# Optimization experiments

Hardware: AMD Instinct MI355X
Metric: run time of the kernel (lower is better)

Reference implementation:

```python
import jax, jax.numpy as jnp
import numpy as np
from jax import lax

B, Ht, Wt, C, NH, KV, FF = 32, 32, 32, 768, 12, 16, 4
HD = C // NH
EPS = 1e-5


def setup_inputs() -> dict:
    key = jax.random.key(0)
    ks = jax.random.split(key, 12)
    rn = lambda k, s, sc=0.02: jax.random.normal(k, s, jnp.float32) * sc
    inp = {"x": jax.random.normal(ks[0], (B, Ht * Wt, C), jnp.float32)}
    inp["ln1_g"] = jnp.ones((C,), jnp.float32)
    inp["ln1_b"] = jnp.zeros((C,), jnp.float32)
    for i, nm in enumerate(["q", "k", "v"]):
        inp[f"dw_w_{nm}"] = rn(ks[1 + i], (C, 1, 3, 3), 0.1)
        inp[f"dw_b_{nm}"] = jnp.zeros((C,), jnp.float32)
        inp[f"bn_g_{nm}"] = jnp.ones((C,), jnp.float32)
        inp[f"bn_b_{nm}"] = jnp.zeros((C,), jnp.float32)
        inp[f"bn_m_{nm}"] = jnp.zeros((C,), jnp.float32)
        inp[f"bn_v_{nm}"] = jnp.ones((C,), jnp.float32)
        inp[f"W_{nm}"] = rn(ks[4 + i], (C, C))
        inp[f"b_{nm}"] = jnp.zeros((C,), jnp.float32)
    inp["ln2_g"] = jnp.ones((C,), jnp.float32)
    inp["ln2_b"] = jnp.zeros((C,), jnp.float32)
    inp["W1"] = rn(ks[7], (FF * C, C))
    inp["b1"] = jnp.zeros((FF * C,), jnp.float32)
    inp["W2"] = rn(ks[8], (C, FF * C))
    inp["b2"] = jnp.zeros((C,), jnp.float32)
    return inp


def _ln(x, g, b):
    m = jnp.mean(x, -1, keepdims=True)
    v = jnp.var(x, -1, keepdims=True)
    return (x - m) * lax.rsqrt(v + EPS) * g + b


def _dw_branch(x4, w, bias, g, bb, m, v, stride):
    # depthwise conv (groups=C) -> ELU -> BatchNorm (eval) -> b (h w) c
    y = lax.conv_general_dilated(
        x4, w, (stride, stride), [(1, 1), (1, 1)],
        feature_group_count=C,
        dimension_numbers=("NCHW", "OIHW", "NCHW"),
    ) + bias[None, :, None, None]
    y = jax.nn.elu(y)
    y = (y - m[None, :, None, None]) * lax.rsqrt(v + EPS)[None, :, None, None] \
        * g[None, :, None, None] + bb[None, :, None, None]
    return y.reshape(B, C, -1).transpose(0, 2, 1)  # (B, n, C)


def _heads(t, Wm, bm):
    t = t @ Wm.T + bm                         # (B, n, C)
    n = t.shape[1]
    return t.reshape(B, n, NH, HD).transpose(0, 2, 1, 3)  # (B, H, n, d)


def reference(x, ln1_g, ln1_b,
              dw_w_q, dw_b_q, bn_g_q, bn_b_q, bn_m_q, bn_v_q, W_q, b_q,
              dw_w_k, dw_b_k, bn_g_k, bn_b_k, bn_m_k, bn_v_k, W_k, b_k,
              dw_w_v, dw_b_v, bn_g_v, bn_b_v, bn_m_v, bn_v_v, W_v, b_v,
              ln2_g, ln2_b, W1, b1, W2, b2):
    xn = _ln(x, ln1_g, ln1_b)
    x4 = xn.transpose(0, 2, 1).reshape(B, C, Ht, Wt)
    q = _heads(_dw_branch(x4, dw_w_q, dw_b_q, bn_g_q, bn_b_q, bn_m_q, bn_v_q, 1), W_q, b_q)
    k = _heads(_dw_branch(x4, dw_w_k, dw_b_k, bn_g_k, bn_b_k, bn_m_k, bn_v_k, 2), W_k, b_k)
    v = _heads(_dw_branch(x4, dw_w_v, dw_b_v, bn_g_v, bn_b_v, bn_m_v, bn_v_v, 2), W_v, b_v)
    scale = 1.0 / (HD ** 0.5)
    attn = jnp.einsum("bhnd,bhmd->bhnm", q, k) * scale
    attn = jax.nn.softmax(attn, axis=-1)
    o = jnp.einsum("bhnm,bhmd->bhnd", attn, v)
    o = o.transpose(0, 2, 1, 3).reshape(B, Ht * Wt, C)
    x = x + o  # DropPath is identity at inference
    h = _ln(x, ln2_g, ln2_b)
    h = jax.nn.gelu(h @ W1.T + b1, approximate=False) @ W2.T + b2
    return x + h
```

## Files before the change

kernel.cpp:

```cpp
#include <hip/hip_runtime.h>
#include <math.h>

#define NB   32
#define C_   768
#define NQ   1024
#define NKV  256
#define NH_  12
#define HD_  64
#define FFC  3072
#define EPS_ 1e-5f

typedef __attribute__((ext_vector_type(8))) _Float16 f16x8;
typedef __attribute__((ext_vector_type(4))) _Float16 f16x4;
typedef __attribute__((ext_vector_type(2))) _Float16 f16x2;
typedef __attribute__((ext_vector_type(4))) float    f32x4;

__device__ __forceinline__ void gload_lds16(const void* g, void* l) {
  __builtin_amdgcn_global_load_lds((const __attribute__((address_space(1))) void*)g,
                                   (__attribute__((address_space(3))) void*)l, 16, 0, 0);
}

__device__ __forceinline__ float gelu_f(float x) {
  return x / (1.f + __expf(-1.5957691216f * (x + 0.044715f * x * x * x)));
}

__global__ __launch_bounds__(256)
void ln_fwd_kernel(const float* __restrict__ x, const float* __restrict__ g,
                   const float* __restrict__ b, _Float16* __restrict__ out) {
  const int row = blockIdx.x;
  const float* xr = x + (size_t)row * C_;
  const int t = threadIdx.x;
  float v0 = xr[t], v1 = xr[t + 256], v2 = xr[t + 512];
  float s = v0 + v1 + v2;
  float q = v0 * v0 + v1 * v1 + v2 * v2;
#pragma unroll
  for (int m = 1; m < 64; m <<= 1) { s += __shfl_xor(s, m); q += __shfl_xor(q, m); }
  __shared__ float ls[4], lq[4];
  const int w = t >> 6, lane = t & 63;
  if (lane == 0) { ls[w] = s; lq[w] = q; }
  __syncthreads();
  s = ls[0] + ls[1] + ls[2] + ls[3];
  q = lq[0] + lq[1] + lq[2] + lq[3];
  const float mean = s * (1.f / C_);
  const float rstd = rsqrtf(q * (1.f / C_) - mean * mean + EPS_);
  _Float16* orow = out + (size_t)row * C_;
  orow[t]       = (_Float16)((v0 - mean) * rstd * g[t]       + b[t]);
  orow[t + 256] = (_Float16)((v1 - mean) * rstd * g[t + 256] + b[t + 256]);
  orow[t + 512] = (_Float16)((v2 - mean) * rstd * g[t + 512] + b[t + 512]);
}

__global__ __launch_bounds__(256)
void resln2_kernel(const float* __restrict__ x, const _Float16* __restrict__ o,
                   const float* __restrict__ g, const float* __restrict__ bb,
                   float* __restrict__ xr_out, _Float16* __restrict__ h) {
  const int row = blockIdx.x;
  const float* xp = x + (size_t)row * C_;
  const _Float16* op = o + (size_t)row * C_;
  const int t = threadIdx.x;
  float v[3]; float s = 0.f, q = 0.f;
#pragma unroll
  for (int i = 0; i < 3; i++) {
    int c = t + i * 256;
    v[i] = xp[c] + (float)op[c];
    s += v[i]; q += v[i] * v[i];
  }
#pragma unroll
  for (int m = 1; m < 64; m <<= 1) { s += __shfl_xor(s, m); q += __shfl_xor(q, m); }
  __shared__ float ls[4], lq[4];
  const int w = t >> 6, lane = t & 63;
  if (lane == 0) { ls[w] = s; lq[w] = q; }
  __syncthreads();
  s = ls[0] + ls[1] + ls[2] + ls[3];
  q = lq[0] + lq[1] + lq[2] + lq[3];
  const float mean = s * (1.f / C_);
  const float rstd = rsqrtf(q * (1.f / C_) - mean * mean + EPS_);
#pragma unroll
  for (int i = 0; i < 3; i++) {
    int c = t + i * 256;
    xr_out[(size_t)row * C_ + c] = v[i];
    h[(size_t)row * C_ + c] = (_Float16)((v[i] - mean) * rstd * g[c] + bb[c]);
  }
}

#define SZ_CC (C_ * C_)
#define SZ_CF (FFC * C_)
__global__ void cast_all_kernel(const float* __restrict__ Wq, const float* __restrict__ Wk,
                                const float* __restrict__ Wv, const float* __restrict__ W1,
                                const float* __restrict__ W2,
                                _Float16* __restrict__ oq, _Float16* __restrict__ ok,
                                _Float16* __restrict__ ov, _Float16* __restrict__ o1,
                                _Float16* __restrict__ o2) {
  const int total = 3 * SZ_CC + 2 * SZ_CF;
  int i = blockIdx.x * 256 + threadIdx.x;
  int stride = gridDim.x * 256;
  for (; i < total; i += stride) {
    if (i < SZ_CC)                     oq[i] = (_Float16)Wq[i];
    else if (i < 2 * SZ_CC)            ok[i - SZ_CC] = (_Float16)Wk[i - SZ_CC];
    else if (i < 3 * SZ_CC)            ov[i - 2 * SZ_CC] = (_Float16)Wv[i - 2 * SZ_CC];
    else if (i < 3 * SZ_CC + SZ_CF)    o1[i - 3 * SZ_CC] = (_Float16)W1[i - 3 * SZ_CC];
    else                               o2[i - 3 * SZ_CC - SZ_CF] = (_Float16)W2[i - 3 * SZ_CC - SZ_CF];
  }
}

__global__ __launch_bounds__(256)
void vtrans_kernel(const _Float16* __restrict__ vbuf, _Float16* __restrict__ vT) {
  const int b = blockIdx.z;
  const int c = blockIdx.y * 256 + threadIdx.x;
  const int kvb = blockIdx.x * 64;
#pragma unroll
  for (int kk = 0; kk < 8; kk++) {
    int kv0 = kvb + kk * 8;
    f16x8 v;
#pragma unroll
    for (int j = 0; j < 8; j++)
      v[j] = vbuf[(size_t)((b << 8) + kv0 + j) * C_ + c];
    *(f16x8*)(vT + ((size_t)(b * C_ + c) << 8) + kv0) = v;
  }
}

struct DwP { const float *w, *bias, *g, *b, *m, *v; };

__device__ __forceinline__ float elu_f(float x) {
  return x > 0.f ? x : __expf(x) - 1.f;
}

__global__ __launch_bounds__(384)
void dw_fused_kernel(const _Float16* __restrict__ xn, DwP pq, DwP pk, DwP pv,
                     _Float16* __restrict__ oq, _Float16* __restrict__ ok,
                     _Float16* __restrict__ ov) {
  const int i = blockIdx.x;
  const int jh = blockIdx.y;
  const int b = blockIdx.z;
  const int c0 = 2 * threadIdx.x;
  const _Float16* xb = xn + (size_t)b * NQ * C_ + c0;

  float wqx[9], wqy[9], wkx[9], wky[9], wvx[9], wvy[9];
#pragma unroll
  for (int u = 0; u < 9; u++) {
    wqx[u] = pq.w[c0 * 9 + u]; wqy[u] = pq.w[(c0 + 1) * 9 + u];
    wkx[u] = pk.w[c0 * 9 + u]; wky[u] = pk.w[(c0 + 1) * 9 + u];
    wvx[u] = pv.w[c0 * 9 + u]; wvy[u] = pv.w[(c0 + 1) * 9 + u];
  }
  const float skqx = rsqrtf(pq.v[c0] + EPS_) * pq.g[c0], bnqx = pq.b[c0] - pq.m[c0] * skqx;
  const float skqy = rsqrtf(pq.v[c0+1] + EPS_) * pq.g[c0+1], bnqy = pq.b[c0+1] - pq.m[c0+1] * skqy;
  const float skkx = rsqrtf(pk.v[c0] + EPS_) * pk.g[c0], bnkx = pk.b[c0] - pk.m[c0] * skkx;
  const float skky = rsqrtf(pk.v[c0+1] + EPS_) * pk.g[c0+1], bnky = pk.b[c0+1] - pk.m[c0+1] * skky;
  const float skvx = rsqrtf(pv.v[c0] + EPS_) * pv.g[c0], bnvx = pv.b[c0] - pv.m[c0] * skvx;
  const float skvy = rsqrtf(pv.v[c0+1] + EPS_) * pv.g[c0+1], bnvy = pv.b[c0+1] - pv.m[c0+1] * skvy;
  const float cbqx = pq.bias[c0], cbqy = pq.bias[c0+1];
  const float cbkx = pk.bias[c0], cbky = pk.bias[c0+1];
  const float cbvx = pv.bias[c0], cbvy = pv.bias[c0+1];

  float tx[5][5], ty[5][5];
  auto ldc = [&](int s, int iw) {
    const bool cv = (iw >= 0 && iw < 32);
#pragma unroll
    for (int u = 0; u < 5; u++) {
      int ih = 2 * i - 1 + u;
      if (cv && ih >= 0 && ih < 32) {
        f16x2 p = *(const f16x2*)&xb[(size_t)(ih * 32 + iw) * C_];
        tx[u][s] = (float)p[0]; ty[u][s] = (float)p[1];
      } else { tx[u][s] = 0.f; ty[u][s] = 0.f; }
    }
  };

  const int j0 = jh * 8;
#pragma unroll
  for (int jj = 0; jj < 8; jj++) {
    const int j = j0 + jj;
    if (jj == 0) {
      ldc(0, 2 * j0 - 1); ldc(1, 2 * j0); ldc(2, 2 * j0 + 1);
      ldc(3, 2 * j0 + 2); ldc(4, 2 * j0 + 3);
    } else {
#pragma unroll
      for (int u = 0; u < 5; u++) {
        tx[u][0] = tx[u][2]; tx[u][1] = tx[u][3]; tx[u][2] = tx[u][4];
        ty[u][0] = ty[u][2]; ty[u][1] = ty[u][3]; ty[u][2] = ty[u][4];
      }
      ldc(3, 2 * j + 2); ldc(4, 2 * j + 3);
    }
    float akx = cbkx, aky = cbky, avx = cbvx, avy = cbvy;
#pragma unroll
    for (int u = 0; u < 3; u++)
#pragma unroll
      for (int vv = 0; vv < 3; vv++) {
        akx += tx[u][vv] * wkx[u * 3 + vv]; aky += ty[u][vv] * wky[u * 3 + vv];
        avx += tx[u][vv] * wvx[u * 3 + vv]; avy += ty[u][vv] * wvy[u * 3 + vv];
      }
    f16x2 kv2, vv2;
    kv2[0] = (_Float16)(elu_f(akx) * skkx + bnkx);
    kv2[1] = (_Float16)(elu_f(aky) * skky + bnky);
    vv2[0] = (_Float16)(elu_f(avx) * skvx + bnvx);
    vv2[1] = (_Float16)(elu_f(avy) * skvy + bnvy);
    *(f16x2*)&ok[((size_t)b * NKV + i * 16 + j) * C_ + c0] = kv2;
    *(f16x2*)&ov[((size_t)b * NKV + i * 16 + j) * C_ + c0] = vv2;
#pragma unroll
    for (int a = 0; a < 2; a++)
#pragma unroll
      for (int b2 = 0; b2 < 2; b2++) {
        float aqx = cbqx, aqy = cbqy;
#pragma unroll
        for (int u = 0; u < 3; u++)
#pragma unroll
          for (int vv = 0; vv < 3; vv++) {
            aqx += tx[a + u][b2 + vv] * wqx[u * 3 + vv];
            aqy += ty[a + u][b2 + vv] * wqy[u * 3 + vv];
          }
        f16x2 q2;
        q2[0] = (_Float16)(elu_f(aqx) * skqx + bnqx);
        q2[1] = (_Float16)(elu_f(aqy) * skqy + bnqy);
        *(f16x2*)&oq[((size_t)b * NQ + (2 * i + a) * 32 + (2 * j + b2)) * C_ + c0] = q2;
      }
  }
}

__device__ __forceinline__ void stage_tile(const _Float16* __restrict__ src, int ldk,
                                           int row0, int kt, _Float16* lds, int w, int lane) {
#pragma unroll
  for (int it = 0; it < 4; it++) {
    int cid = (it * 4 + w) * 64 + lane;
    int row = cid >> 3, kg = cid & 7;
    int kgs = kg ^ (row & 7);
    const _Float16* g = src + (size_t)(row0 + row) * ldk + kt * 64 + kgs * 8;
    gload_lds16((const void*)g, (void*)((char*)lds + (it * 4 + w) * 1024));
  }
}

__device__ __forceinline__
void gemm_core128(const _Float16* __restrict__ A, const _Float16* __restrict__ Bw,
                  const float* __restrict__ bias, _Float16* __restrict__ outh,
                  int N, int K, int m0, int n0) {
  __shared__ __align__(16) _Float16 As[128 * 64];
  __shared__ __align__(16) _Float16 Bs[128 * 64];
  const int tid = threadIdx.x, w = tid >> 6, lane = tid & 63;
  const int wm = w >> 1, wn = w & 1;

  f32x4 acc[4][4];
#pragma unroll
  for (int i = 0; i < 4; i++)
#pragma unroll
    for (int j = 0; j < 4; j++)
#pragma unroll
      for (int r = 0; r < 4; r++) acc[i][j][r] = 0.f;

  const int NKT = K >> 6;
  for (int kt = 0; kt < NKT; kt++) {
    stage_tile(A, K, m0, kt, As, w, lane);
    stage_tile(Bw, K, n0, kt, Bs, w, lane);
    __syncthreads();
    f16x8 af[4][2], bfr[4][2];
#pragma unroll
    for (int mi = 0; mi < 4; mi++)
#pragma unroll
      for (int kh = 0; kh < 2; kh++) {
        int row = wm * 64 + mi * 16 + (lane & 15);
        int kg = kh * 4 + (lane >> 4);
        af[mi][kh] = *(const f16x8*)&As[row * 64 + ((kg ^ (row & 7)) << 3)];
      }
#pragma unroll
    for (int ni = 0; ni < 4; ni++)
#pragma unroll
      for (int kh = 0; kh < 2; kh++) {
        int row = wn * 64 + ni * 16 + (lane & 15);
        int kg = kh * 4 + (lane >> 4);
        bfr[ni][kh] = *(const f16x8*)&Bs[row * 64 + ((kg ^ (row & 7)) << 3)];
      }
    __builtin_amdgcn_s_setprio(1);
#pragma unroll
    for (int mi = 0; mi < 4; mi++)
#pragma unroll
      for (int ni = 0; ni < 4; ni++)
#pragma unroll
        for (int kh = 0; kh < 2; kh++)
          acc[mi][ni] = __builtin_amdgcn_mfma_f32_16x16x32_f16(af[mi][kh], bfr[ni][kh],
                                                               acc[mi][ni], 0, 0, 0);
    __builtin_amdgcn_s_setprio(0);
    __syncthreads();
  }
#pragma unroll
  for (int mi = 0; mi < 4; mi++)
#pragma unroll
    for (int ni = 0; ni < 4; ni++) {
      int col = n0 + wn * 64 + ni * 16 + (lane & 15);
      float bv = bias[col];
#pragma unroll
      for (int r = 0; r < 4; r++) {
        int rowg = m0 + wm * 64 + mi * 16 + (lane >> 4) * 4 + r;
        outh[(size_t)rowg * N + col] = (_Float16)(acc[mi][ni][r] + bv);
      }
    }
}

__global__ __launch_bounds__(256, 3)
void gemm_q(const _Float16* __restrict__ A, const _Float16* __restrict__ Bw,
            const float* __restrict__ bias, _Float16* __restrict__ outh,
            int N, int K, int NT) {
  const int nwg = gridDim.x, d = blockIdx.x;
  const int o = (d & 7) * (nwg >> 3) + (d >> 3);
  gemm_core128(A, Bw, bias, outh, N, K, (o / NT) * 128, (o % NT) * 128);
}

__global__ __launch_bounds__(256, 3)
void gemm_kv(const _Float16* __restrict__ Ak, const _Float16* __restrict__ Wk,
             const float* __restrict__ bk, _Float16* __restrict__ outk,
             const _Float16* __restrict__ Av, const _Float16* __restrict__ Wv,
             const float* __restrict__ bv, _Float16* __restrict__ outv) {
  const int nwg = gridDim.x, d = blockIdx.x;
  int o = (d & 7) * (nwg >> 3) + (d >> 3);
  const bool isv = o >= 384;
  if (isv) o -= 384;
  const int m0 = (o / 6) * 128, n0 = (o % 6) * 128;
  if (isv) gemm_core128(Av, Wv, bv, outv, C_, C_, m0, n0);
  else     gemm_core128(Ak, Wk, bk, outk, C_, C_, m0, n0);
}

__device__ __forceinline__ void stage256(const _Float16* __restrict__ src, int ldk,
                                         int row0, int kt, _Float16* lds, int w, int lane) {
#pragma unroll
  for (int it = 0; it < 4; it++) {
    int cid = it * 512 + w * 64 + lane;
    int row = cid >> 3, kg = cid & 7;
    const _Float16* g = src + (size_t)(row0 + row) * ldk + kt * 64 + ((kg ^ (row & 7)) << 3);
    gload_lds16((const void*)g, (void*)((char*)lds + (it * 512 + w * 64) * 16));
  }
}

template <int EPI>
__global__ __launch_bounds__(512, 2)
void gemm256(const _Float16* __restrict__ A, const _Float16* __restrict__ Bw,
             const float* __restrict__ bias,
             _Float16* __restrict__ outh, float* __restrict__ outf,
             int N, int K, int NT) {
  __shared__ __align__(16) _Float16 As[2][256 * 64];
  __shared__ __align__(16) _Float16 Bs[2][256 * 64];
  const int tid = threadIdx.x, w = tid >> 6, lane = tid & 63;
  const int wm = w >> 2, wn = w & 3;
  const int hi = lane >> 4, lo = lane & 15;
  const int nwg = gridDim.x, d = blockIdx.x;
  const int o = (d & 7) * (nwg >> 3) + (d >> 3);
  const int m0 = (o / NT) * 256, n0 = (o % NT) * 256;

  f32x4 acc[8][4];
#pragma unroll
  for (int i = 0; i < 8; i++)
#pragma unroll
    for (int j = 0; j < 4; j++)
#pragma unroll
      for (int r = 0; r < 4; r++) acc[i][j][r] = 0.f;

  stage256(A, K, m0, 0, As[0], w, lane);
  stage256(Bw, K, n0, 0, Bs[0], w, lane);
  stage256(A, K, m0, 1, As[1], w, lane);
  stage256(Bw, K, n0, 1, Bs[1], w, lane);
  asm volatile("s_waitcnt vmcnt(8)" ::: "memory");
  __builtin_amdgcn_s_barrier();

  const int NKT = K >> 6;
  int cur = 0;
  for (int kt = 0; kt < NKT; kt++) {
    const _Float16* as = As[cur];
    const _Float16* bs = Bs[cur];
#pragma unroll
    for (int mh = 0; mh < 2; mh++)
#pragma unroll
      for (int nh = 0; nh < 2; nh++) {
        f16x8 af[4][2], bf[2][2];
#pragma unroll
        for (int mi = 0; mi < 4; mi++)
#pragma unroll
          for (int kh = 0; kh < 2; kh++) {
            int row = wm * 128 + mh * 64 + mi * 16 + lo;
            int kg = kh * 4 + hi;
            af[mi][kh] = *(const f16x8*)&as[row * 64 + ((kg ^ (row & 7)) << 3)];
          }
#pragma unroll
        for (int ni = 0; ni < 2; ni++)
#pragma unroll
          for (int kh = 0; kh < 2; kh++) {
            int row = wn * 64 + nh * 32 + ni * 16 + lo;
            int kg = kh * 4 + hi;
            bf[ni][kh] = *(const f16x8*)&bs[row * 64 + ((kg ^ (row & 7)) << 3)];
          }
        __builtin_amdgcn_s_setprio(1);
#pragma unroll
        for (int mi = 0; mi < 4; mi++)
#pragma unroll
          for (int ni = 0; ni < 2; ni++)
#pragma unroll
            for (int kh = 0; kh < 2; kh++)
              acc[mh * 4 + mi][nh * 2 + ni] =
                  __builtin_amdgcn_mfma_f32_16x16x32_f16(af[mi][kh], bf[ni][kh],
                                                         acc[mh * 4 + mi][nh * 2 + ni], 0, 0, 0);
        __builtin_amdgcn_s_setprio(0);
        __builtin_amdgcn_sched_barrier(0);
      }
    __builtin_amdgcn_s_barrier();
    if (kt + 2 < NKT) {
      stage256(A, K, m0, kt + 2, As[cur], w, lane);
      stage256(Bw, K, n0, kt + 2, Bs[cur], w, lane);
      asm volatile("s_waitcnt vmcnt(8)" ::: "memory");
    } else {
      asm volatile("s_waitcnt vmcnt(0)" ::: "memory");
    }
    __builtin_amdgcn_s_barrier();
    cur ^= 1;
  }
#pragma unroll
  for (int mh = 0; mh < 2; mh++)
#pragma unroll
    for (int mi = 0; mi < 4; mi++)
#pragma unroll
      for (int nh = 0; nh < 2; nh++)
#pragma unroll
        for (int ni = 0; ni < 2; ni++) {
          int col = n0 + wn * 64 + nh * 32 + ni * 16 + lo;
          float bv = bias[col];
#pragma unroll
          for (int r = 0; r < 4; r++) {
            int rowg = m0 + wm * 128 + mh * 64 + mi * 16 + hi * 4 + r;
            float val = acc[mh * 4 + mi][nh * 2 + ni][r] + bv;
            size_t idx = (size_t)rowg * N + col;
            if (EPI == 1) outh[idx] = (_Float16)gelu_f(val);
            else          outf[idx] += val;
          }
        }
}

__global__ __launch_bounds__(512, 2)
void attn_kernel(const _Float16* __restrict__ Q, const _Float16* __restrict__ Kb,
                 const _Float16* __restrict__ vT, _Float16* __restrict__ O) {
  __shared__ __align__(16) _Float16 Klds[256 * 64];
  __shared__ __align__(16) _Float16 Vt[64 * 256];
  const int tid = threadIdx.x, w = tid >> 6, lane = tid & 63;
  const int hi = lane >> 4, lo = lane & 15;
  const int half = blockIdx.x & 1;
  const int h = (blockIdx.x >> 1) % NH_;
  const int b = blockIdx.x / (2 * NH_);

  const _Float16* qp = Q + (size_t)b * NQ * C_ + h * HD_;
  const _Float16* kp = Kb + (size_t)b * NKV * C_ + h * HD_;
  const _Float16* vp = vT + ((size_t)(b * C_ + h * HD_) << 8);

#pragma unroll
  for (int i = 0; i < 4; i++) {
    int cid = i * 512 + w * 64 + lane;
    int row = cid >> 3, kg = cid & 7;
    const _Float16* g = kp + (size_t)row * C_ + ((kg ^ (row & 7)) << 3);
    gload_lds16((const void*)g, (void*)((char*)Klds + (i * 512 + w * 64) * 16));
  }
#pragma unroll
  for (int i = 0; i < 4; i++) {
    int cid = i * 512 + w * 64 + lane;
    int row = cid >> 5, kg = cid & 31;
    const _Float16* g = vp + ((size_t)row << 8) + ((kg ^ (row & 7)) << 3);
    gload_lds16((const void*)g, (void*)((char*)Vt + (i * 512 + w * 64) * 16));
  }
  __syncthreads();

#pragma unroll
  for (int ti = 0; ti < 4; ti++) {
    const int q0 = half * 512 + w * 64 + ti * 16;
    f16x8 qf[2];
#pragma unroll
    for (int kh = 0; kh < 2; kh++)
      qf[kh] = *(const f16x8*)(qp + (size_t)(q0 + lo) * C_ + kh * 32 + hi * 8);
    f32x4 S[16];
#pragma unroll
    for (int nt = 0; nt < 16; nt++) {
      f32x4 s; s[0] = 0.f; s[1] = 0.f; s[2] = 0.f; s[3] = 0.f;
      const _Float16* krow = &Klds[(nt * 16 + lo) * 64];
#pragma unroll
      for (int kh = 0; kh < 2; kh++) {
        f16x8 kf = *(const f16x8*)&krow[((kh * 4 + hi) ^ (lo & 7)) << 3];
        s = __builtin_amdgcn_mfma_f32_16x16x32_f16(kf, qf[kh], s, 0, 0, 0);
      }
      S[nt] = s;
    }
    float mx = -1e30f;
#pragma unroll
    for (int nt = 0; nt < 16; nt++)
#pragma unroll
      for (int r = 0; r < 4; r++) { S[nt][r] *= 0.125f; mx = fmaxf(mx, S[nt][r]); }
    mx = fmaxf(mx, __shfl_xor(mx, 16));
    mx = fmaxf(mx, __shfl_xor(mx, 32));
    float sum = 0.f;
#pragma unroll
    for (int nt = 0; nt < 16; nt++)
#pragma unroll
      for (int r = 0; r < 4; r++) { float e = __expf(S[nt][r] - mx); S[nt][r] = e; sum += e; }
    sum += __shfl_xor(sum, 16);
    sum += __shfl_xor(sum, 32);
    const float inv = 1.f / sum;
    f16x8 pa8[8];
#pragma unroll
    for (int ntp = 0; ntp < 8; ntp++)
#pragma unroll
      for (int r = 0; r < 4; r++) {
        pa8[ntp][r]     = (_Float16)(S[2 * ntp][r] * inv);
        pa8[ntp][4 + r] = (_Float16)(S[2 * ntp + 1][r] * inv);
      }
    f32x4 acc[4];
#pragma unroll
    for (int dt = 0; dt < 4; dt++) { acc[dt][0] = 0.f; acc[dt][1] = 0.f; acc[dt][2] = 0.f; acc[dt][3] = 0.f; }
#pragma unroll
    for (int dt = 0; dt < 4; dt++) {
      const int d = dt * 16 + lo, sw = d & 7;
      const _Float16* vrow = &Vt[d * 256 + 4 * (hi & 1)];
#pragma unroll
      for (int ntp = 0; ntp < 8; ntp++) {
        f16x4 v0 = *(const f16x4*)&vrow[((4 * ntp + (hi >> 1)) ^ sw) << 3];
        f16x4 v1 = *(const f16x4*)&vrow[((4 * ntp + 2 + (hi >> 1)) ^ sw) << 3];
        f16x8 vt8;
#pragma unroll
        for (int r = 0; r < 4; r++) { vt8[r] = v0[r]; vt8[4 + r] = v1[r]; }
        acc[dt] = __builtin_amdgcn_mfma_f32_16x16x32_f16(pa8[ntp], vt8, acc[dt], 0, 0, 0);
      }
    }
#pragma unroll
    for (int dt = 0; dt < 4; dt++)
#pragma unroll
      for (int r = 0; r < 4; r++)
        O[(size_t)(b * NQ + q0 + 4 * hi + r) * C_ + h * HD_ + dt * 16 + lo] = (_Float16)acc[dt][r];
  }
}

extern "C" void kernel_launch(void* const* d_in, const int* in_sizes, int n_in,
                              void* d_out, int out_size, void* d_ws, size_t ws_size,
                              hipStream_t stream) {
  (void)in_sizes; (void)n_in; (void)out_size; (void)ws_size;
  const float* x    = (const float*)d_in[0];
  const float* ln1g = (const float*)d_in[1];
  const float* ln1b = (const float*)d_in[2];
  DwP pq { (const float*)d_in[3], (const float*)d_in[4], (const float*)d_in[5],
           (const float*)d_in[6], (const float*)d_in[7], (const float*)d_in[8] };
  const float* Wq = (const float*)d_in[9];  const float* bq = (const float*)d_in[10];
  DwP pk { (const float*)d_in[11], (const float*)d_in[12], (const float*)d_in[13],
           (const float*)d_in[14], (const float*)d_in[15], (const float*)d_in[16] };
  const float* Wk = (const float*)d_in[17]; const float* bk = (const float*)d_in[18];
  DwP pv { (const float*)d_in[19], (const float*)d_in[20], (const float*)d_in[21],
           (const float*)d_in[22], (const float*)d_in[23], (const float*)d_in[24] };
  const float* Wv = (const float*)d_in[25]; const float* bv = (const float*)d_in[26];
  const float* ln2g = (const float*)d_in[27];
  const float* ln2b = (const float*)d_in[28];
  const float* W1 = (const float*)d_in[29]; const float* b1 = (const float*)d_in[30];
  const float* W2 = (const float*)d_in[31]; const float* b2 = (const float*)d_in[32];

  char* ws = (char*)d_ws;
  _Float16* gbuf = (_Float16*)(ws + 0);
  _Float16* xn   = (_Float16*)(ws + 0);
  _Float16* qb   = (_Float16*)(ws + 50331648);
  _Float16* tk   = (_Float16*)(ws + 100663296);
  _Float16* tv   = (_Float16*)(ws + 113246208);
  _Float16* vTb  = tv;
  _Float16* kb   = (_Float16*)(ws + 125829120);
  _Float16* vbuf = (_Float16*)(ws + 138412032);
  _Float16* o    = (_Float16*)(ws + 150994944);
  _Float16* tq   = (_Float16*)(ws + 201326592);
  _Float16* hb   = tq;
  _Float16* wqh  = (_Float16*)(ws + 251658240);
  _Float16* wkh  = (_Float16*)(ws + 252837888);
  _Float16* wvh  = (_Float16*)(ws + 254017536);
  _Float16* w1h  = (_Float16*)(ws + 255197184);
  _Float16* w2h  = (_Float16*)(ws + 259915776);
  float* out = (float*)d_out;

  ln_fwd_kernel<<<NB * NQ, 256, 0, stream>>>(x, ln1g, ln1b, xn);
  cast_all_kernel<<<2048, 256, 0, stream>>>(Wq, Wk, Wv, W1, W2, wqh, wkh, wvh, w1h, w2h);
  dw_fused_kernel<<<dim3(16, 2, NB), 384, 0, stream>>>(xn, pq, pk, pv, tq, tk, tv);
  gemm_q<<<1536, 256, 0, stream>>>(tq, wqh, bq, qb, C_, C_, 6);
  gemm_kv<<<768, 256, 0, stream>>>(tk, wkh, bk, kb, tv, wvh, bv, vbuf);
  vtrans_kernel<<<dim3(4, 3, NB), 256, 0, stream>>>(vbuf, vTb);
  attn_kernel<<<NB * NH_ * 2, 512, 0, stream>>>(qb, kb, vTb, o);
  resln2_kernel<<<NB * NQ, 256, 0, stream>>>(x, o, ln2g, ln2b, out, hb);
  gemm256<1><<<1536, 512, 0, stream>>>(hb, w1h, b1, gbuf, nullptr, FFC, C_, 12);
  gemm256<2><<<384, 512, 0, stream>>>(gbuf, w2h, b2, nullptr, out, C_, FFC, 3);
}
```

Before: 967.1 us.

## Triple-buffer FFN GEMMs with 256x128 tiles and split depthwise conv grid

The FFN GEMMs move from 256x256 double-buffered tiles to 256x128 tiles with a three-stage LDS ring. Loads for tile kt+2 are issued before computing tile kt, which removes one barrier per iteration and doubles the grid so more workgroups are available. The depthwise conv kernel also splits its columns into four chunks of 4 instead of two of 8, for more blocks at the cost of more halo reloads. Smaller N tiles lower per-block arithmetic intensity and raise total global traffic for the A operand.

Result: slower. 992.6 us (+2.6%).

```diff
diff --git a/kernel.cpp b/kernel.cpp
--- a/kernel.cpp
+++ b/kernel.cpp
@@ -129,7 +129,7 @@
                      _Float16* __restrict__ oq, _Float16* __restrict__ ok,
                      _Float16* __restrict__ ov) {
   const int i = blockIdx.x;
-  const int jh = blockIdx.y;
+  const int jq = blockIdx.y;
   const int b = blockIdx.z;
   const int c0 = 2 * threadIdx.x;
   const _Float16* xb = xn + (size_t)b * NQ * C_ + c0;
@@ -164,9 +164,9 @@
     }
   };
 
-  const int j0 = jh * 8;
-#pragma unroll
-  for (int jj = 0; jj < 8; jj++) {
+  const int j0 = jq * 4;
+#pragma unroll
+  for (int jj = 0; jj < 4; jj++) {
     const int j = j0 + jj;
     if (jj == 0) {
       ldc(0, 2 * j0 - 1); ldc(1, 2 * j0); ldc(2, 2 * j0 + 1);
@@ -314,116 +314,145 @@
   else     gemm_core128(Ak, Wk, bk, outk, C_, C_, m0, n0);
 }
 
-__device__ __forceinline__ void stage256(const _Float16* __restrict__ src, int ldk,
-                                         int row0, int kt, _Float16* lds, int w, int lane) {
+__device__ __forceinline__ void stageA256(const _Float16* __restrict__ src, int ldk,
+                                          int row0, int kt, _Float16* lds, int w, int lane,
+                                          int tid) {
 #pragma unroll
   for (int it = 0; it < 4; it++) {
-    int cid = it * 512 + w * 64 + lane;
+    int cid = it * 512 + tid;
     int row = cid >> 3, kg = cid & 7;
     const _Float16* g = src + (size_t)(row0 + row) * ldk + kt * 64 + ((kg ^ (row & 7)) << 3);
     gload_lds16((const void*)g, (void*)((char*)lds + (it * 512 + w * 64) * 16));
   }
 }
+__device__ __forceinline__ void stageB128(const _Float16* __restrict__ src, int ldk,
+                                          int row0, int kt, _Float16* lds, int w, int lane,
+                                          int tid) {
+#pragma unroll
+  for (int it = 0; it < 2; it++) {
+    int cid = it * 512 + tid;
+    int row = cid >> 3, kg = cid & 7;
+    const _Float16* g = src + (size_t)(row0 + row) * ldk + kt * 64 + ((kg ^ (row & 7)) << 3);
+    gload_lds16((const void*)g, (void*)((char*)lds + (it * 512 + w * 64) * 16));
+  }
+}
 
 template <int EPI>
 __global__ __launch_bounds__(512, 2)
-void gemm256(const _Float16* __restrict__ A, const _Float16* __restrict__ Bw,
-             const float* __restrict__ bias,
-             _Float16* __restrict__ outh, float* __restrict__ outf,
-             int N, int K, int NT) {
-  __shared__ __align__(16) _Float16 As[2][256 * 64];
-  __shared__ __align__(16) _Float16 Bs[2][256 * 64];
+void gemm_pipe(const _Float16* __restrict__ A, const _Float16* __restrict__ Bw,
+               const float* __restrict__ bias,
+               _Float16* __restrict__ outh, float* __restrict__ outf,
+               int N, int K, int NT) {
+  __shared__ __align__(16) _Float16 As[3][256 * 64];
+  __shared__ __align__(16) _Float16 Bs[3][128 * 64];
   const int tid = threadIdx.x, w = tid >> 6, lane = tid & 63;
-  const int wm = w >> 2, wn = w & 3;
+  const int wm = w >> 1, wn = w & 1;
   const int hi = lane >> 4, lo = lane & 15;
   const int nwg = gridDim.x, d = blockIdx.x;
   const int o = (d & 7) * (nwg >> 3) + (d >> 3);
-  const int m0 = (o / NT) * 256, n0 = (o % NT) * 256;
-
-  f32x4 acc[8][4];
-#pragma unroll
-  for (int i = 0; i < 8; i++)
+  const int m0 = (o / NT) * 256, n0 = (o % NT) * 128;
+
+  f32x4 acc[4][4];
+#pragma unroll
+  for (int i = 0; i < 4; i++)
 #pragma unroll
     for (int j = 0; j < 4; j++)
 #pragma unroll
       for (int r = 0; r < 4; r++) acc[i][j][r] = 0.f;
 
-  stage256(A, K, m0, 0, As[0], w, lane);
-  stage256(Bw, K, n0, 0, Bs[0], w, lane);
-  stage256(A, K, m0, 1, As[1], w, lane);
-  stage256(Bw, K, n0, 1, Bs[1], w, lane);
-  asm volatile("s_waitcnt vmcnt(8)" ::: "memory");
+  const int NKT = K >> 6;
+  stageA256(A, K, m0, 0, As[0], w, lane, tid);
+  stageB128(Bw, K, n0, 0, Bs[0], w, lane, tid);
+  stageA256(A, K, m0, 1, As[1], w, lane, tid);
+  stageB128(Bw, K, n0, 1, Bs[1], w, lane, tid);
+  asm volatile("s_waitcnt vmcnt(6)" ::: "memory");
   __builtin_amdgcn_s_barrier();
-
-  const int NKT = K >> 6;
-  int cur = 0;
+  asm volatile("" ::: "memory");
+
+  int rc = 0, rs = 2;
   for (int kt = 0; kt < NKT; kt++) {
-    const _Float16* as = As[cur];
-    const _Float16* bs = Bs[cur];
-#pragma unroll
-    for (int mh = 0; mh < 2; mh++)
-#pragma unroll
-      for (int nh = 0; nh < 2; nh++) {
-        f16x8 af[4][2], bf[2][2];
-#pragma unroll
-        for (int mi = 0; mi < 4; mi++)
-#pragma unroll
-          for (int kh = 0; kh < 2; kh++) {
-            int row = wm * 128 + mh * 64 + mi * 16 + lo;
-            int kg = kh * 4 + hi;
-            af[mi][kh] = *(const f16x8*)&as[row * 64 + ((kg ^ (row & 7)) << 3)];
-          }
+    if (kt + 2 < NKT) {
+      stageA256(A, K, m0, kt + 2, As[rs], w, lane, tid);
+      stageB128(Bw, K, n0, kt + 2, Bs[rs], w, lane, tid);
+    }
+    const _Float16* as = As[rc];
+    const _Float16* bs = Bs[rc];
+    f16x8 af[4][2];
+#pragma unroll
+    for (int mi = 0; mi < 4; mi++)
+#pragma unroll
+      for (int kh = 0; kh < 2; kh++) {
+        int row = wm * 64 + mi * 16 + lo;
+        int kg = kh * 4 + hi;
+        af[mi][kh] = *(const f16x8*)&as[row * 64 + ((kg ^ (row & 7)) << 3)];
+      }
+    {
+      f16x8 bf[2][2];
+#pragma unroll
+      for (int ni = 0; ni < 2; ni++)
+#pragma unroll
+        for (int kh = 0; kh < 2; kh++) {
+          int row = wn * 64 + ni * 16 + lo;
+          int kg = kh * 4 + hi;
+          bf[ni][kh] = *(const f16x8*)&bs[row * 64 + ((kg ^ (row & 7)) << 3)];
+        }
+      __builtin_amdgcn_s_setprio(1);
+#pragma unroll
+      for (int mi = 0; mi < 4; mi++)
 #pragma unroll
         for (int ni = 0; ni < 2; ni++)
 #pragma unroll
-          for (int kh = 0; kh < 2; kh++) {
-            int row = wn * 64 + nh * 32 + ni * 16 + lo;
-            int kg = kh * 4 + hi;
-            bf[ni][kh] = *(const f16x8*)&bs[row * 64 + ((kg ^ (row & 7)) << 3)];
-          }
-        __builtin_amdgcn_s_setprio(1);
-#pragma unroll
-        for (int mi = 0; mi < 4; mi++)
-#pragma unroll
-          for (int ni = 0; ni < 2; ni++)
-#pragma unroll
-            for (int kh = 0; kh < 2; kh++)
-              acc[mh * 4 + mi][nh * 2 + ni] =
-                  __builtin_amdgcn_mfma_f32_16x16x32_f16(af[mi][kh], bf[ni][kh],
-                                                         acc[mh * 4 + mi][nh * 2 + ni], 0, 0, 0);
-        __builtin_amdgcn_s_setprio(0);
-        __builtin_amdgcn_sched_barrier(0);
-      }
-    __builtin_amdgcn_s_barrier();
+          for (int kh = 0; kh < 2; kh++)
+            acc[mi][ni] = __builtin_amdgcn_mfma_f32_16x16x32_f16(af[mi][kh], bf[ni][kh],
+                                                                 acc[mi][ni], 0, 0, 0);
+      __builtin_amdgcn_s_setprio(0);
+    }
+    {
+      f16x8 bf[2][2];
+#pragma unroll
+      for (int ni = 0; ni < 2; ni++)
+#pragma unroll
+        for (int kh = 0; kh < 2; kh++) {
+          int row = wn * 64 + (ni + 2) * 16 + lo;
+          int kg = kh * 4 + hi;
+          bf[ni][kh] = *(const f16x8*)&bs[row * 64 + ((kg ^ (row & 7)) << 3)];
+        }
+      __builtin_amdgcn_s_setprio(1);
+#pragma unroll
+      for (int mi = 0; mi < 4; mi++)
+#pragma unroll
+        for (int ni = 0; ni < 2; ni++)
+#pragma unroll
+          for (int kh = 0; kh < 2; kh++)
+            acc[mi][ni + 2] = __builtin_amdgcn_mfma_f32_16x16x32_f16(af[mi][kh], bf[ni][kh],
+                                                                     acc[mi][ni + 2], 0, 0, 0);
+      __builtin_amdgcn_s_setprio(0);
+    }
     if (kt + 2 < NKT) {
-      stage256(A, K, m0, kt + 2, As[cur], w, lane);
-      stage256(Bw, K, n0, kt + 2, Bs[cur], w, lane);
-      asm volatile("s_waitcnt vmcnt(8)" ::: "memory");
+      asm volatile("s_waitcnt vmcnt(6)" ::: "memory");
     } else {
       asm volatile("s_waitcnt vmcnt(0)" ::: "memory");
     }
     __builtin_amdgcn_s_barrier();
-    cur ^= 1;
-  }
-#pragma unroll
-  for (int mh = 0; mh < 2; mh++)
-#pragma unroll
-    for (int mi = 0; mi < 4; mi++)
-#pragma unroll
-      for (int nh = 0; nh < 2; nh++)
-#pragma unroll
-        for (int ni = 0; ni < 2; ni++) {
-          int col = n0 + wn * 64 + nh * 32 + ni * 16 + lo;
-          float bv = bias[col];
-#pragma unroll
-          for (int r = 0; r < 4; r++) {
-            int rowg = m0 + wm * 128 + mh * 64 + mi * 16 + hi * 4 + r;
-            float val = acc[mh * 4 + mi][nh * 2 + ni][r] + bv;
-            size_t idx = (size_t)rowg * N + col;
-            if (EPI == 1) outh[idx] = (_Float16)gelu_f(val);
-            else          outf[idx] += val;
-          }
-        }
+    asm volatile("" ::: "memory");
+    rc = (rc == 2) ? 0 : rc + 1;
+    rs = (rs == 2) ? 0 : rs + 1;
+  }
+#pragma unroll
+  for (int mi = 0; mi < 4; mi++)
+#pragma unroll
+    for (int ni = 0; ni < 4; ni++) {
+      int col = n0 + wn * 64 + ni * 16 + lo;
+      float bv = bias[col];
+#pragma unroll
+      for (int r = 0; r < 4; r++) {
+        int rowg = m0 + wm * 64 + mi * 16 + hi * 4 + r;
+        float val = acc[mi][ni][r] + bv;
+        size_t idx = (size_t)rowg * N + col;
+        if (EPI == 1) outh[idx] = (_Float16)gelu_f(val);
+        else          outf[idx] += val;
+      }
+    }
 }
 
 __global__ __launch_bounds__(512, 2)
@@ -566,12 +595,12 @@
 
   ln_fwd_kernel<<<NB * NQ, 256, 0, stream>>>(x, ln1g, ln1b, xn);
   cast_all_kernel<<<2048, 256, 0, stream>>>(Wq, Wk, Wv, W1, W2, wqh, wkh, wvh, w1h, w2h);
-  dw_fused_kernel<<<dim3(16, 2, NB), 384, 0, stream>>>(xn, pq, pk, pv, tq, tk, tv);
+  dw_fused_kernel<<<dim3(16, 4, NB), 384, 0, stream>>>(xn, pq, pk, pv, tq, tk, tv);
   gemm_q<<<1536, 256, 0, stream>>>(tq, wqh, bq, qb, C_, C_, 6);
   gemm_kv<<<768, 256, 0, stream>>>(tk, wkh, bk, kb, tv, wvh, bv, vbuf);
   vtrans_kernel<<<dim3(4, 3, NB), 256, 0, stream>>>(vbuf, vTb);
   attn_kernel<<<NB * NH_ * 2, 512, 0, stream>>>(qb, kb, vTb, o);
   resln2_kernel<<<NB * NQ, 256, 0, stream>>>(x, o, ln2g, ln2b, out, hb);
-  gemm256<1><<<1536, 512, 0, stream>>>(hb, w1h, b1, gbuf, nullptr, FFC, C_, 12);
-  gemm256<2><<<384, 512, 0, stream>>>(gbuf, w2h, b2, nullptr, out, C_, FFC, 3);
-}
+  gemm_pipe<1><<<3072, 512, 0, stream>>>(hb, w1h, b1, gbuf, nullptr, FFC, C_, 24);
+  gemm_pipe<2><<<768, 512, 0, stream>>>(gbuf, w2h, b2, nullptr, out, C_, FFC, 6);
+}
```
